# Kernel tuning notes

Hardware: AMD Instinct MI355X
Metric: run time of the kernel (lower is better)

Reference implementation:

```python
import jax, jax.numpy as jnp
import numpy as np

N = 8192

def setup_inputs() -> dict:
    key = jax.random.key(0)
    k1, k2, k3, k4, k5 = jax.random.split(key, 5)
    adj = jax.random.uniform(k1, (N, N), dtype=jnp.float32)
    W1 = jax.random.normal(k2, (2, 64), dtype=jnp.float32) * 0.5
    b1 = jax.random.normal(k3, (64,), dtype=jnp.float32) * 0.1
    W2 = jax.random.normal(k4, (64, 64), dtype=jnp.float32) * 0.1
    b2 = jax.random.normal(k5, (64,), dtype=jnp.float32) * 0.1
    return {"adj": adj, "W1": W1, "b1": b1, "W2": W2, "b2": b2}

def reference(adj, W1, b1, W2, b2):
    n = adj.shape[0]
    # node features: [ones, deg / max(deg clamped to >=1)]
    deg = adj.sum(axis=1)                                  # (n,)
    deg_norm = deg / jnp.maximum(jnp.max(jnp.maximum(deg, 1.0)), 1.0)
    x = jnp.stack([jnp.ones(n, dtype=adj.dtype), deg_norm], axis=1)  # (n,2)
    # A_norm = D^-1/2 (A+I) D^-1/2, expressed as row/col elementwise scaling
    a = adj + jnp.eye(n, dtype=adj.dtype)
    d_inv_sqrt = jnp.power(jnp.maximum(a.sum(axis=1), 1.0), -0.5)    # (n,)
    a_norm = d_inv_sqrt[:, None] * a * d_inv_sqrt[None, :]           # (n,n)
    # two dense GCN layers
    h = jax.nn.relu((a_norm @ x) @ W1 + b1)                # (n,64)
    h = (a_norm @ h) @ W2 + b2                             # (n,64)
    return h
```

## Files before the change

### kernel.cpp

```cpp
#include <hip/hip_runtime.h>
#include <stdint.h>

#define N 8192
#define KSPLIT 8
#define BK 64
#define KPB (N / KSPLIT)
#define TILES (KPB / BK)

typedef __attribute__((ext_vector_type(8))) short sh8;
typedef __attribute__((ext_vector_type(4))) float f32x4;
typedef __attribute__((ext_vector_type(2))) float f32x2;

static __device__ __forceinline__ unsigned short f2bf(float f) {
    union { float f; unsigned u; } v; v.f = f;
    unsigned r = v.u + 0x7FFF + ((v.u >> 16) & 1);
    return (unsigned short)(r >> 16);
}

static __device__ __forceinline__ float bflo(unsigned u) {
    union { unsigned u; float f; } v; v.u = u << 16;
    return v.f;
}

static __device__ __forceinline__ float bfhi(unsigned u) {
    union { unsigned u; float f; } v; v.u = u & 0xFFFF0000u;
    return v.f;
}

static __device__ __forceinline__ unsigned fbits(float f) {
    union { float f; unsigned u; } v; v.f = f;
    return v.u;
}

static __device__ __forceinline__ void glds16(const void* g, void* l) {
    __builtin_amdgcn_global_load_lds(
        (const __attribute__((address_space(1))) void*)g,
        (__attribute__((address_space(3))) void*)l, 16, 0, 0);
}

__global__ __launch_bounds__(256) void k_deg_conv(const float* __restrict__ adj,
        unsigned char* __restrict__ abf, float* __restrict__ deg) {
    int row = blockIdx.x;
    const float* arow = adj + (size_t)row * N;
    unsigned* brow = (unsigned*)(abf + (size_t)row * N);
    int t = threadIdx.x;
    float sum = 0.f;
    #pragma unroll
    for (int it = 0; it < N / 1024; ++it) {
        int j = (it * 256 + t) * 4;
        float4 v = *(const float4*)(arow + j);
        sum += v.x + v.y + v.z + v.w;
        int d = row - j;
        float x0 = v.x + ((d == 0) ? 1.f : 0.f);
        float x1 = v.y + ((d == 1) ? 1.f : 0.f);
        float x2 = v.z + ((d == 2) ? 1.f : 0.f);
        float x3 = v.w + ((d == 3) ? 1.f : 0.f);
        unsigned p = __builtin_amdgcn_cvt_pk_fp8_f32(x0, x1, 0, false);
        p = __builtin_amdgcn_cvt_pk_fp8_f32(x2, x3, p, true);
        brow[it * 256 + t] = p;
    }
    __shared__ float red[256];
    red[t] = sum; __syncthreads();
    for (int sz = 128; sz > 0; sz >>= 1) {
        if (t < sz) red[t] += red[t + sz];
        __syncthreads();
    }
    if (t == 0) deg[row] = red[0];
}

__global__ __launch_bounds__(1024) void k_scalars(const float* __restrict__ deg,
        float* __restrict__ s, unsigned* __restrict__ yb) {
    __shared__ float red[1024];
    int t = threadIdx.x;
    float m = 1.0f;
    for (int i = t; i < N; i += 1024) m = fmaxf(m, deg[i]);
    red[t] = m; __syncthreads();
    for (int sz = 512; sz > 0; sz >>= 1) {
        if (t < sz) red[t] = fmaxf(red[t], red[t + sz]);
        __syncthreads();
    }
    float gmax = red[0];
    for (int i = t; i < N; i += 1024) {
        float d = deg[i];
        float si = 1.0f / sqrtf(fmaxf(d + 1.0f, 1.0f));
        s[i] = si;
        unsigned lo = f2bf(si);
        unsigned hi = f2bf(si * (d / gmax));
        yb[i] = (hi << 16) | lo;
    }
}

__global__ __launch_bounds__(256) void k_layer1(const unsigned char* __restrict__ abf,
        const unsigned* __restrict__ yb, const float* __restrict__ s,
        const float* __restrict__ W1, const float* __restrict__ b1,
        unsigned short* __restrict__ gT) {
    int wave = threadIdx.x >> 6;
    int lane = threadIdx.x & 63;
    int row = blockIdx.x * 4 + wave;
    const unsigned char* arow = abf + (size_t)row * N;
    float z0 = 0.f, z1 = 0.f;
    #pragma unroll 4
    for (int it = 0; it < N / 512; ++it) {
        int j = it * 512 + lane * 8;
        uint2 a8 = *(const uint2*)(arow + j);
        uint4 w0 = *(const uint4*)(yb + j);
        uint4 w1 = *(const uint4*)(yb + j + 4);
        f32x2 c01 = __builtin_amdgcn_cvt_pk_f32_fp8((int)a8.x, false);
        f32x2 c23 = __builtin_amdgcn_cvt_pk_f32_fp8((int)a8.x, true);
        f32x2 c45 = __builtin_amdgcn_cvt_pk_f32_fp8((int)a8.y, false);
        f32x2 c67 = __builtin_amdgcn_cvt_pk_f32_fp8((int)a8.y, true);
        z0 += c01.x * bflo(w0.x) + c01.y * bflo(w0.y)
            + c23.x * bflo(w0.z) + c23.y * bflo(w0.w)
            + c45.x * bflo(w1.x) + c45.y * bflo(w1.y)
            + c67.x * bflo(w1.z) + c67.y * bflo(w1.w);
        z1 += c01.x * bfhi(w0.x) + c01.y * bfhi(w0.y)
            + c23.x * bfhi(w0.z) + c23.y * bfhi(w0.w)
            + c45.x * bfhi(w1.x) + c45.y * bfhi(w1.y)
            + c67.x * bfhi(w1.z) + c67.y * bfhi(w1.w);
    }
    #pragma unroll
    for (int m = 1; m < 64; m <<= 1) {
        z0 += __shfl_xor(z0, m);
        z1 += __shfl_xor(z1, m);
    }
    float si = s[row];
    float h = si * (z0 * W1[lane] + z1 * W1[64 + lane]) + b1[lane];
    h = fmaxf(h, 0.f);
    gT[(size_t)lane * N + row] = f2bf(si * h);
}

__global__ __launch_bounds__(256) void k_layer2a(const unsigned char* __restrict__ abf,
        const unsigned short* __restrict__ gT, float* __restrict__ tpart) {
    __shared__ unsigned char  Al[2][64 * 64];
    __shared__ unsigned short Bl[2][64 * 64];
    int tid = threadIdx.x;
    int wave = tid >> 6, lane = tid & 63;
    int r0 = blockIdx.x * 64;
    int kbase0 = blockIdx.y * KPB;

    int r = lane & 15, q = lane >> 4;

    f32x4 acc0 = {0,0,0,0}, acc1 = {0,0,0,0}, acc2 = {0,0,0,0}, acc3 = {0,0,0,0};

    #define STAGE(buf, kbase)                                                   \
        do {                                                                    \
            {                                                                   \
                int idx = tid;                                                  \
                int srow = idx >> 2, sch = (idx & 3) ^ (srow & 3);              \
                glds16(abf + (size_t)(r0 + srow) * N + (kbase) + sch * 16,      \
                       &Al[buf][idx * 16]);                                     \
            }                                                                   \
            _Pragma("unroll")                                                   \
            for (int i = 0; i < 2; ++i) {                                       \
                int idx = i * 256 + tid;                                        \
                int srow = idx >> 3, sch = (idx & 7) ^ (srow & 7);              \
                glds16(gT + (size_t)srow * N + (kbase) + sch * 8,               \
                       &Bl[buf][idx * 8]);                                      \
            }                                                                   \
        } while (0)

    STAGE(0, kbase0);
    __syncthreads();

    for (int t = 0; t < TILES; ++t) {
        int cur = t & 1;
        if (t + 1 < TILES) STAGE(cur ^ 1, kbase0 + (t + 1) * BK);
        int arow = wave * 16 + r;
        #pragma unroll
        for (int ks = 0; ks < 2; ++ks) {
            int acho = (((ks * 2 + (q >> 1)) ^ (arow & 3)) * 16) + (q & 1) * 8;
            uint2 a8 = *(const uint2*)&Al[cur][arow * 64 + acho];
            f32x2 c01 = __builtin_amdgcn_cvt_pk_f32_fp8((int)a8.x, false);
            f32x2 c23 = __builtin_amdgcn_cvt_pk_f32_fp8((int)a8.x, true);
            f32x2 c45 = __builtin_amdgcn_cvt_pk_f32_fp8((int)a8.y, false);
            f32x2 c67 = __builtin_amdgcn_cvt_pk_f32_fp8((int)a8.y, true);
            union { unsigned u[4]; sh8 v; } af;
            af.u[0] = (fbits(c01.y) & 0xFFFF0000u) | (fbits(c01.x) >> 16);
            af.u[1] = (fbits(c23.y) & 0xFFFF0000u) | (fbits(c23.x) >> 16);
            af.u[2] = (fbits(c45.y) & 0xFFFF0000u) | (fbits(c45.x) >> 16);
            af.u[3] = (fbits(c67.y) & 0xFFFF0000u) | (fbits(c67.x) >> 16);
            int chb = ((ks * 4 + q) ^ (r & 7)) * 8;
            sh8 b0 = *(const sh8*)&Bl[cur][(r     ) * 64 + chb];
            sh8 b1 = *(const sh8*)&Bl[cur][(r + 16) * 64 + chb];
            sh8 b2 = *(const sh8*)&Bl[cur][(r + 32) * 64 + chb];
            sh8 b3 = *(const sh8*)&Bl[cur][(r + 48) * 64 + chb];
            acc0 = __builtin_amdgcn_mfma_f32_16x16x32_bf16(af.v, b0, acc0, 0, 0, 0);
            acc1 = __builtin_amdgcn_mfma_f32_16x16x32_bf16(af.v, b1, acc1, 0, 0, 0);
            acc2 = __builtin_amdgcn_mfma_f32_16x16x32_bf16(af.v, b2, acc2, 0, 0, 0);
            acc3 = __builtin_amdgcn_mfma_f32_16x16x32_bf16(af.v, b3, acc3, 0, 0, 0);
        }
        __syncthreads();
    }
    #undef STAGE

    float* tp = tpart + (size_t)blockIdx.y * N * 64;
    int growb = r0 + wave * 16 + q * 4;
    #pragma unroll
    for (int rr = 0; rr < 4; ++rr) {
        tp[(size_t)(growb + rr) * 64 + r     ] = acc0[rr];
        tp[(size_t)(growb + rr) * 64 + r + 16] = acc1[rr];
        tp[(size_t)(growb + rr) * 64 + r + 32] = acc2[rr];
        tp[(size_t)(growb + rr) * 64 + r + 48] = acc3[rr];
    }
}

__global__ __launch_bounds__(256) void k_layer2b(const float* __restrict__ tpart,
        const float* __restrict__ s, const float* __restrict__ W2,
        const float* __restrict__ b2, float* __restrict__ out) {
    __shared__ float ts[4][64];
    int tid = threadIdx.x;
    int r0 = blockIdx.x * 4;
    int rg = tid >> 6, c = tid & 63;
    float v = 0.f;
    #pragma unroll
    for (int kb = 0; kb < KSPLIT; ++kb)
        v += tpart[(size_t)kb * N * 64 + (size_t)(r0 + rg) * 64 + c];
    ts[rg][c] = v;
    __syncthreads();
    float acc = 0.f;
    #pragma unroll 8
    for (int cc = 0; cc < 64; ++cc)
        acc += ts[rg][cc] * W2[cc * 64 + c];
    int row = r0 + rg;
    out[(size_t)row * 64 + c] = s[row] * acc + b2[c];
}

extern "C" void kernel_launch(void* const* d_in, const int* in_sizes, int n_in,
                              void* d_out, int out_size, void* d_ws, size_t ws_size,
                              hipStream_t stream) {
    const float* adj = (const float*)d_in[0];
    const float* W1  = (const float*)d_in[1];
    const float* b1  = (const float*)d_in[2];
    const float* W2  = (const float*)d_in[3];
    const float* b2  = (const float*)d_in[4];
    float* out = (float*)d_out;

    char* ws = (char*)d_ws;
    unsigned char*  abf = (unsigned char*)ws;
    unsigned short* gT  = (unsigned short*)(ws + (size_t)N * N);
    float* tpart = (float*)(ws + (size_t)N * N + (size_t)64 * N * 2);
    float* deg = tpart + (size_t)KSPLIT * N * 64;
    float* s   = deg + N;
    unsigned* yb = (unsigned*)(s + N);

    hipLaunchKernelGGL(k_deg_conv, dim3(N),      dim3(256),  0, stream, adj, abf, deg);
    hipLaunchKernelGGL(k_scalars,  dim3(1),      dim3(1024), 0, stream, deg, s, yb);
    hipLaunchKernelGGL(k_layer1,   dim3(N / 4),  dim3(256),  0, stream, abf, yb, s, W1, b1, gT);
    hipLaunchKernelGGL(k_layer2a,  dim3(N / 64, KSPLIT), dim3(256), 0, stream, abf, gT, tpart);
    hipLaunchKernelGGL(k_layer2b,  dim3(N / 4),  dim3(256),  0, stream, tpart, s, W2, b2, out);
}
```

Measured before the change: 118.2 us.

## Fold scalar kernel into degree pass via last-block atomic counter

The single-block scalars kernel is removed. The last block of the degree/conversion kernel, detected with an atomic counter, now computes the global max and the packed yb vector. Downstream kernels recompute the inverse square root from deg instead of reading a stored s array. The block reduction now uses wave shuffles, and the bf16 packing in layer2a uses a byte-permute instruction. This saves one launch and a serialized tiny kernel, at the cost of an extra memset and a serial tail on the last block.

```diff
diff --git a/kernel.cpp b/kernel.cpp
--- a/kernel.cpp
+++ b/kernel.cpp
@@ -39,11 +39,15 @@
 }
 
 __global__ __launch_bounds__(256) void k_deg_conv(const float* __restrict__ adj,
-        unsigned char* __restrict__ abf, float* __restrict__ deg) {
+        unsigned char* __restrict__ abf, float* __restrict__ deg,
+        unsigned* __restrict__ cnt, unsigned* __restrict__ yb) {
     int row = blockIdx.x;
+    int t = threadIdx.x;
+    int wave = t >> 6, lane = t & 63;
     const float* arow = adj + (size_t)row * N;
     unsigned* brow = (unsigned*)(abf + (size_t)row * N);
-    int t = threadIdx.x;
+    __shared__ float red4[4];
+    __shared__ unsigned lastf;
     float sum = 0.f;
     #pragma unroll
     for (int it = 0; it < N / 1024; ++it) {
@@ -59,31 +63,35 @@
         p = __builtin_amdgcn_cvt_pk_fp8_f32(x2, x3, p, true);
         brow[it * 256 + t] = p;
     }
-    __shared__ float red[256];
-    red[t] = sum; __syncthreads();
-    for (int sz = 128; sz > 0; sz >>= 1) {
-        if (t < sz) red[t] += red[t + sz];
-        __syncthreads();
-    }
-    if (t == 0) deg[row] = red[0];
-}
-
-__global__ __launch_bounds__(1024) void k_scalars(const float* __restrict__ deg,
-        float* __restrict__ s, unsigned* __restrict__ yb) {
-    __shared__ float red[1024];
-    int t = threadIdx.x;
+    #pragma unroll
+    for (int m = 1; m < 64; m <<= 1) sum += __shfl_xor(sum, m);
+    if (lane == 0) red4[wave] = sum;
+    __syncthreads();
+    if (t == 0) {
+        float tot = red4[0] + red4[1] + red4[2] + red4[3];
+        atomicExch(&deg[row], tot);
+        asm volatile("s_waitcnt vmcnt(0)" ::: "memory");
+        lastf = (atomicAdd(cnt, 1u) == (unsigned)(N - 1)) ? 1u : 0u;
+    }
+    __syncthreads();
+    if (lastf == 0) return;
+
     float m = 1.0f;
-    for (int i = t; i < N; i += 1024) m = fmaxf(m, deg[i]);
-    red[t] = m; __syncthreads();
-    for (int sz = 512; sz > 0; sz >>= 1) {
-        if (t < sz) red[t] = fmaxf(red[t], red[t + sz]);
-        __syncthreads();
-    }
-    float gmax = red[0];
-    for (int i = t; i < N; i += 1024) {
-        float d = deg[i];
+    for (int it = 0; it < N / 256; ++it) {
+        float d = __hip_atomic_load(&deg[it * 256 + t],
+                                    __ATOMIC_RELAXED, __HIP_MEMORY_SCOPE_AGENT);
+        m = fmaxf(m, d);
+    }
+    #pragma unroll
+    for (int o = 1; o < 64; o <<= 1) m = fmaxf(m, __shfl_xor(m, o));
+    if (lane == 0) red4[wave] = m;
+    __syncthreads();
+    float gmax = fmaxf(fmaxf(red4[0], red4[1]), fmaxf(red4[2], red4[3]));
+    for (int it = 0; it < N / 256; ++it) {
+        int i = it * 256 + t;
+        float d = __hip_atomic_load(&deg[i],
+                                    __ATOMIC_RELAXED, __HIP_MEMORY_SCOPE_AGENT);
         float si = 1.0f / sqrtf(fmaxf(d + 1.0f, 1.0f));
-        s[i] = si;
         unsigned lo = f2bf(si);
         unsigned hi = f2bf(si * (d / gmax));
         yb[i] = (hi << 16) | lo;
@@ -91,7 +99,7 @@
 }
 
 __global__ __launch_bounds__(256) void k_layer1(const unsigned char* __restrict__ abf,
-        const unsigned* __restrict__ yb, const float* __restrict__ s,
+        const unsigned* __restrict__ yb, const float* __restrict__ deg,
         const float* __restrict__ W1, const float* __restrict__ b1,
         unsigned short* __restrict__ gT) {
     int wave = threadIdx.x >> 6;
@@ -119,11 +127,12 @@
             + c67.x * bfhi(w1.z) + c67.y * bfhi(w1.w);
     }
     #pragma unroll
-    for (int m = 1; m < 64; m <<= 1) {
-        z0 += __shfl_xor(z0, m);
-        z1 += __shfl_xor(z1, m);
-    }
-    float si = s[row];
+    for (int o = 1; o < 64; o <<= 1) {
+        z0 += __shfl_xor(z0, o);
+        z1 += __shfl_xor(z1, o);
+    }
+    float dv = deg[row];
+    float si = 1.0f / sqrtf(fmaxf(dv + 1.0f, 1.0f));
     float h = si * (z0 * W1[lane] + z1 * W1[64 + lane]) + b1[lane];
     h = fmaxf(h, 0.f);
     gT[(size_t)lane * N + row] = f2bf(si * h);
@@ -175,19 +184,19 @@
             f32x2 c45 = __builtin_amdgcn_cvt_pk_f32_fp8((int)a8.y, false);
             f32x2 c67 = __builtin_amdgcn_cvt_pk_f32_fp8((int)a8.y, true);
             union { unsigned u[4]; sh8 v; } af;
-            af.u[0] = (fbits(c01.y) & 0xFFFF0000u) | (fbits(c01.x) >> 16);
-            af.u[1] = (fbits(c23.y) & 0xFFFF0000u) | (fbits(c23.x) >> 16);
-            af.u[2] = (fbits(c45.y) & 0xFFFF0000u) | (fbits(c45.x) >> 16);
-            af.u[3] = (fbits(c67.y) & 0xFFFF0000u) | (fbits(c67.x) >> 16);
+            af.u[0] = __builtin_amdgcn_perm(fbits(c01.y), fbits(c01.x), 0x07060302);
+            af.u[1] = __builtin_amdgcn_perm(fbits(c23.y), fbits(c23.x), 0x07060302);
+            af.u[2] = __builtin_amdgcn_perm(fbits(c45.y), fbits(c45.x), 0x07060302);
+            af.u[3] = __builtin_amdgcn_perm(fbits(c67.y), fbits(c67.x), 0x07060302);
             int chb = ((ks * 4 + q) ^ (r & 7)) * 8;
             sh8 b0 = *(const sh8*)&Bl[cur][(r     ) * 64 + chb];
             sh8 b1 = *(const sh8*)&Bl[cur][(r + 16) * 64 + chb];
-            sh8 b2 = *(const sh8*)&Bl[cur][(r + 32) * 64 + chb];
+            sh8 b2v = *(const sh8*)&Bl[cur][(r + 32) * 64 + chb];
             sh8 b3 = *(const sh8*)&Bl[cur][(r + 48) * 64 + chb];
-            acc0 = __builtin_amdgcn_mfma_f32_16x16x32_bf16(af.v, b0, acc0, 0, 0, 0);
-            acc1 = __builtin_amdgcn_mfma_f32_16x16x32_bf16(af.v, b1, acc1, 0, 0, 0);
-            acc2 = __builtin_amdgcn_mfma_f32_16x16x32_bf16(af.v, b2, acc2, 0, 0, 0);
-            acc3 = __builtin_amdgcn_mfma_f32_16x16x32_bf16(af.v, b3, acc3, 0, 0, 0);
+            acc0 = __builtin_amdgcn_mfma_f32_16x16x32_bf16(af.v, b0,  acc0, 0, 0, 0);
+            acc1 = __builtin_amdgcn_mfma_f32_16x16x32_bf16(af.v, b1,  acc1, 0, 0, 0);
+            acc2 = __builtin_amdgcn_mfma_f32_16x16x32_bf16(af.v, b2v, acc2, 0, 0, 0);
+            acc3 = __builtin_amdgcn_mfma_f32_16x16x32_bf16(af.v, b3,  acc3, 0, 0, 0);
         }
         __syncthreads();
     }
@@ -205,7 +214,7 @@
 }
 
 __global__ __launch_bounds__(256) void k_layer2b(const float* __restrict__ tpart,
-        const float* __restrict__ s, const float* __restrict__ W2,
+        const float* __restrict__ deg, const float* __restrict__ W2,
         const float* __restrict__ b2, float* __restrict__ out) {
     __shared__ float ts[4][64];
     int tid = threadIdx.x;
@@ -222,7 +231,9 @@
     for (int cc = 0; cc < 64; ++cc)
         acc += ts[rg][cc] * W2[cc * 64 + c];
     int row = r0 + rg;
-    out[(size_t)row * 64 + c] = s[row] * acc + b2[c];
+    float dv = deg[row];
+    float si = 1.0f / sqrtf(fmaxf(dv + 1.0f, 1.0f));
+    out[(size_t)row * 64 + c] = si * acc + b2[c];
 }
 
 extern "C" void kernel_launch(void* const* d_in, const int* in_sizes, int n_in,
@@ -240,12 +251,16 @@
     unsigned short* gT  = (unsigned short*)(ws + (size_t)N * N);
     float* tpart = (float*)(ws + (size_t)N * N + (size_t)64 * N * 2);
     float* deg = tpart + (size_t)KSPLIT * N * 64;
-    float* s   = deg + N;
-    unsigned* yb = (unsigned*)(s + N);
-
-    hipLaunchKernelGGL(k_deg_conv, dim3(N),      dim3(256),  0, stream, adj, abf, deg);
-    hipLaunchKernelGGL(k_scalars,  dim3(1),      dim3(1024), 0, stream, deg, s, yb);
-    hipLaunchKernelGGL(k_layer1,   dim3(N / 4),  dim3(256),  0, stream, abf, yb, s, W1, b1, gT);
-    hipLaunchKernelGGL(k_layer2a,  dim3(N / 64, KSPLIT), dim3(256), 0, stream, abf, gT, tpart);
-    hipLaunchKernelGGL(k_layer2b,  dim3(N / 4),  dim3(256),  0, stream, tpart, s, W2, b2, out);
-}
+    unsigned* cnt = (unsigned*)(deg + N);
+    unsigned* yb  = (unsigned*)((char*)cnt + 64);
+
+    hipMemsetAsync(cnt, 0, sizeof(unsigned), stream);
+    hipLaunchKernelGGL(k_deg_conv, dim3(N),     dim3(256), 0, stream,
+                       adj, abf, deg, cnt, yb);
+    hipLaunchKernelGGL(k_layer1,   dim3(N / 4), dim3(256), 0, stream,
+                       abf, yb, deg, W1, b1, gT);
+    hipLaunchKernelGGL(k_layer2a,  dim3(N / 64, KSPLIT), dim3(256), 0, stream,
+                       abf, gT, tpart);
+    hipLaunchKernelGGL(k_layer2b,  dim3(N / 4), dim3(256), 0, stream,
+                       tpart, deg, W2, b2, out);
+}
```

New measurement: 177.3 us. 50.0% more time.
